# Optimization experiments

Hardware: AMD Instinct MI355X
Metric: run time of the kernel (lower is better)

Reference implementation:

```python
import jax, jax.numpy as jnp
import numpy as np

N_NODES = 50000
N_EDGES = 640000
IN_CH = 128
OUT_CH = 128


def setup_inputs() -> dict:
    key = jax.random.key(0)
    k1, k2, k3, k4 = jax.random.split(key, 4)
    x = jax.random.normal(k1, (N_NODES, IN_CH), dtype=jnp.float32)
    edge_index = jax.random.randint(k2, (2, N_EDGES), 0, N_NODES, dtype=jnp.int32)
    # nn.Linear params: W [out, in], b [out]
    bound = 1.0 / np.sqrt(IN_CH)
    W = jax.random.uniform(k3, (OUT_CH, IN_CH), minval=-bound, maxval=bound, dtype=jnp.float32)
    b = jax.random.uniform(k4, (OUT_CH,), minval=-bound, maxval=bound, dtype=jnp.float32)
    return {"x": x, "edge_index": edge_index, "W": W, "b": b}


def reference(x, edge_index, W, b):
    row, col = edge_index[0], edge_index[1]
    num_nodes = x.shape[0]
    # degree of each destination node (clamped to >= 1)
    deg = jax.ops.segment_sum(jnp.ones(row.shape[0], dtype=x.dtype), row,
                              num_segments=num_nodes)
    deg = jnp.maximum(deg, 1.0)
    # gather neighbor features and scatter-add into destinations
    agg = jax.ops.segment_sum(x[col], row, num_segments=num_nodes)
    agg = agg / deg[:, None]
    # residual + linear
    return (x + agg) @ W.T + b
```

## Files before the change

### kernel.cpp

```cpp
#include <hip/hip_runtime.h>

#define N_NODES 50000
#define N_EDGES 640000
#define CH 128
#define NBINS 1563
#define CAPB 16
#define CAP2 2512
#define CAPR 48
#define NTILES 1563
#define FILLB 157

typedef __bf16 bf16_t;
typedef bf16_t bf16x8 __attribute__((ext_vector_type(8)));
typedef float f32x4 __attribute__((ext_vector_type(4)));
typedef unsigned u32x4 __attribute__((ext_vector_type(4)));

__device__ __forceinline__ ushort f2bf(float f) {
  union { float f; unsigned u; } v; v.f = f;
  unsigned r = v.u + 0x7FFFu + ((v.u >> 16) & 1u);
  return (ushort)(r >> 16);
}
__device__ __forceinline__ float bflo(unsigned u) {
  union { unsigned u; float f; } v; v.u = u << 16; return v.f;
}
__device__ __forceinline__ float bfhi(unsigned u) {
  union { unsigned u; float f; } v; v.u = u & 0xFFFF0000u; return v.f;
}
__device__ __forceinline__ unsigned pack2(float lo, float hi) {
  return (unsigned)f2bf(lo) | ((unsigned)f2bf(hi) << 16);
}


__global__ __launch_bounds__(256) void fill_conv(const int* __restrict__ row,
                                                 const int* __restrict__ col,
                                                 unsigned* __restrict__ binArr,
                                                 const float4* __restrict__ x4,
                                                 uint4* __restrict__ xb4,
                                                 const float4* __restrict__ W4,
                                                 uint4* __restrict__ Wb4) {
  int bid = blockIdx.x;
  int tid = threadIdx.x;
  if (bid < FILLB) {
    __shared__ int lh[NBINS];
    for (int i = tid; i < NBINS; i += 256) lh[i] = 0;
    __syncthreads();
    int base = bid * 4096 + tid * 16;
    bool act = base < N_EDGES;
    int rr[16], cc[16], bi[16], rk[16];
    if (act) {
#pragma unroll
      for (int u = 0; u < 4; ++u) {
        int4 r4 = *(const int4*)(row + base + u * 4);
        int4 c4 = *(const int4*)(col + base + u * 4);
        rr[u * 4 + 0] = r4.x; rr[u * 4 + 1] = r4.y; rr[u * 4 + 2] = r4.z; rr[u * 4 + 3] = r4.w;
        cc[u * 4 + 0] = c4.x; cc[u * 4 + 1] = c4.y; cc[u * 4 + 2] = c4.z; cc[u * 4 + 3] = c4.w;
      }
#pragma unroll
      for (int i = 0; i < 16; ++i) {
        bi[i] = rr[i] >> 5;
        rk[i] = atomicAdd(&lh[bi[i]], 1);
      }
#pragma unroll
      for (int i = 0; i < 16; ++i) {
        if (rk[i] < CAPB) {
          binArr[bi[i] * CAP2 + bid * CAPB + rk[i]] =
              ((unsigned)(rr[i] & 31) << 16) | (unsigned)cc[i];
        }
      }
    }
  } else if (bid < FILLB + 3125) {
    int i = (bid - FILLB) * 256 + tid;
    float4 a = x4[i * 2], b = x4[i * 2 + 1];
    uint4 o;
    o.x = pack2(a.x, a.y); o.y = pack2(a.z, a.w);
    o.z = pack2(b.x, b.y); o.w = pack2(b.z, b.w);
    xb4[i] = o;
  } else {
    for (int i = tid; i < 2048; i += 256) {
      float4 c = W4[i * 2], d = W4[i * 2 + 1];
      uint4 w;
      w.x = pack2(c.x, c.y); w.y = pack2(c.z, c.w);
      w.z = pack2(d.x, d.y); w.w = pack2(d.z, d.w);
      Wb4[i] = w;
    }
  }
}

__global__ __launch_bounds__(256) void fused(const uint4* __restrict__ xb4,
                                             const uint4* __restrict__ binArr4,
                                             const uint4* __restrict__ Wb4,
                                             const float4* __restrict__ bias4,
                                             float4* __restrict__ out4) {
  __shared__ ushort hT[32 * CH];
  __shared__ ushort colL[32 * CAPR];
  __shared__ int rowcnt[32];
  int tid = threadIdx.x;
  int g = blockIdx.x;
  int m0 = g * 32;

  if (tid < 32) rowcnt[tid] = 0;
  __syncthreads();
  {
    const u32x4* seg4 = (const u32x4*)(binArr4 + g * (CAP2 / 4));
    for (int j = tid; j < CAP2 / 4; j += 256) {
      u32x4 rv = __builtin_nontemporal_load(seg4 + j);
      unsigned recs[4] = {rv.x, rv.y, rv.z, rv.w};
#pragma unroll
      for (int i = 0; i < 4; ++i) {
        unsigned rec = recs[i];
        if ((rec >> 21) == 0u) {
          int lr = (rec >> 16) & 31;
          int p = atomicAdd(&rowcnt[lr], 1);
          if (p < CAPR) colL[lr * CAPR + p] = (ushort)(rec & 0xFFFFu);
        }
      }
    }
  }
  __syncthreads();

  int wv = tid >> 6;
  int lane = tid & 63;
  int q = lane & 15;
  int grp = lane >> 4;
#pragma unroll
  for (int t = 0; t < 2; ++t) {
    int r = wv * 8 + t * 4 + grp;
    int node = m0 + r;
    int deg = rowcnt[r];
    int degc = deg < CAPR ? deg : CAPR;
    const ushort* arow = colL + r * CAPR;
    float acc[8] = {0.f, 0.f, 0.f, 0.f, 0.f, 0.f, 0.f, 0.f};
    int e = 0;
    for (; e + 3 < degc; e += 4) {
      uint2 ids = *(const uint2*)(arow + e);
      int n0 = ids.x & 0xFFFF, n1 = ids.x >> 16;
      int n2 = ids.y & 0xFFFF, n3 = ids.y >> 16;
      uint4 v0 = xb4[n0 * 16 + q];
      uint4 v1 = xb4[n1 * 16 + q];
      uint4 v2 = xb4[n2 * 16 + q];
      uint4 v3 = xb4[n3 * 16 + q];
      acc[0] += bflo(v0.x); acc[1] += bfhi(v0.x); acc[2] += bflo(v0.y); acc[3] += bfhi(v0.y);
      acc[4] += bflo(v0.z); acc[5] += bfhi(v0.z); acc[6] += bflo(v0.w); acc[7] += bfhi(v0.w);
      acc[0] += bflo(v1.x); acc[1] += bfhi(v1.x); acc[2] += bflo(v1.y); acc[3] += bfhi(v1.y);
      acc[4] += bflo(v1.z); acc[5] += bfhi(v1.z); acc[6] += bflo(v1.w); acc[7] += bfhi(v1.w);
      acc[0] += bflo(v2.x); acc[1] += bfhi(v2.x); acc[2] += bflo(v2.y); acc[3] += bfhi(v2.y);
      acc[4] += bflo(v2.z); acc[5] += bfhi(v2.z); acc[6] += bflo(v2.w); acc[7] += bfhi(v2.w);
      acc[0] += bflo(v3.x); acc[1] += bfhi(v3.x); acc[2] += bflo(v3.y); acc[3] += bfhi(v3.y);
      acc[4] += bflo(v3.z); acc[5] += bfhi(v3.z); acc[6] += bflo(v3.w); acc[7] += bfhi(v3.w);
    }
    for (; e < degc; ++e) {
      int nb = arow[e];
      uint4 v = xb4[nb * 16 + q];
      acc[0] += bflo(v.x); acc[1] += bfhi(v.x); acc[2] += bflo(v.y); acc[3] += bfhi(v.y);
      acc[4] += bflo(v.z); acc[5] += bfhi(v.z); acc[6] += bflo(v.w); acc[7] += bfhi(v.w);
    }
    uint4 o = make_uint4(0, 0, 0, 0);
    if (node < N_NODES) {
      float s = 1.0f / fmaxf((float)deg, 1.0f);
      uint4 xi = xb4[node * 16 + q];
      o.x = pack2(bflo(xi.x) + acc[0] * s, bfhi(xi.x) + acc[1] * s);
      o.y = pack2(bflo(xi.y) + acc[2] * s, bfhi(xi.y) + acc[3] * s);
      o.z = pack2(bflo(xi.z) + acc[4] * s, bfhi(xi.z) + acc[5] * s);
      o.w = pack2(bflo(xi.w) + acc[6] * s, bfhi(xi.w) + acc[7] * s);
    }
    *(uint4*)&hT[r * CH + ((q ^ (r & 15)) << 3)] = o;
  }
  __syncthreads();

  int qq = grp;
  int mt = wv & 1;
  int nbase = (wv >> 1) * 4;
  const ushort* hbase = &hT[(mt * 16 + q) * CH];
  bf16x8 hb0 = *(const bf16x8*)(hbase + (((qq + 0) ^ q) << 3));
  bf16x8 hb1 = *(const bf16x8*)(hbase + (((qq + 4) ^ q) << 3));
  bf16x8 hb2 = *(const bf16x8*)(hbase + (((qq + 8) ^ q) << 3));
  bf16x8 hb3 = *(const bf16x8*)(hbase + (((qq + 12) ^ q) << 3));
  int m = m0 + mt * 16 + q;
#pragma unroll
  for (int i = 0; i < 4; ++i) {
    int nt = nbase + i;
    const uint4* wr = Wb4 + (nt * 16 + q) * 16 + qq;
    bf16x8 w0 = __builtin_bit_cast(bf16x8, wr[0]);
    bf16x8 w1 = __builtin_bit_cast(bf16x8, wr[4]);
    bf16x8 w2 = __builtin_bit_cast(bf16x8, wr[8]);
    bf16x8 w3 = __builtin_bit_cast(bf16x8, wr[12]);
    f32x4 acc = {0.f, 0.f, 0.f, 0.f};
    acc = __builtin_amdgcn_mfma_f32_16x16x32_bf16(w0, hb0, acc, 0, 0, 0);
    acc = __builtin_amdgcn_mfma_f32_16x16x32_bf16(w1, hb1, acc, 0, 0, 0);
    acc = __builtin_amdgcn_mfma_f32_16x16x32_bf16(w2, hb2, acc, 0, 0, 0);
    acc = __builtin_amdgcn_mfma_f32_16x16x32_bf16(w3, hb3, acc, 0, 0, 0);
    if (m < N_NODES) {
      float4 bv = bias4[nt * 4 + qq];
      f32x4 o;
      o.x = acc[0] + bv.x;
      o.y = acc[1] + bv.y;
      o.z = acc[2] + bv.z;
      o.w = acc[3] + bv.w;
      __builtin_nontemporal_store(o, (f32x4*)(out4 + (size_t)m * 32 + nt * 4 + qq));
    }
  }
}

extern "C" void kernel_launch(void* const* d_in, const int* in_sizes, int n_in,
                              void* d_out, int out_size, void* d_ws, size_t ws_size,
                              hipStream_t stream) {
  const float* x  = (const float*)d_in[0];
  const int*   ei = (const int*)d_in[1];
  const float* W  = (const float*)d_in[2];
  const float* bb = (const float*)d_in[3];

  char* ws = (char*)d_ws;
  unsigned* binArr = (unsigned*)ws;
  uint4*    Wb4    = (uint4*)(ws + 15705024);
  uint4*    xb4    = (uint4*)(ws + 15737792);

  fill_conv<<<FILLB + 3125 + 1, 256, 0, stream>>>(ei, ei + N_EDGES, binArr,
                                                  (const float4*)x, xb4,
                                                  (const float4*)W, Wb4);
  fused<<<NTILES, 256, 0, stream>>>(xb4, (const uint4*)binArr, Wb4,
                                    (const float4*)bb, (float4*)d_out);
}
```

Baseline: 130.3 us.

## Replace fixed-capacity edge binning with atomic-count CSR build and scan

Builds a CSR adjacency via per-node atomic degree counting, a single-block prefix scan, and an atomic scatter of column ids, replacing fixed-capacity bins. The fused kernel then loads just the contiguous column ids for its 32-row tile instead of scanning a padded bin of records. This removes the large padded bin read and the per-row capacity limits, but adds three extra kernel launches, a serial single-block scan, and two passes of global atomics.

```diff
diff --git a/kernel.cpp b/kernel.cpp
--- a/kernel.cpp
+++ b/kernel.cpp
@@ -3,17 +3,12 @@
 #define N_NODES 50000
 #define N_EDGES 640000
 #define CH 128
-#define NBINS 1563
-#define CAPB 16
-#define CAP2 2512
-#define CAPR 48
 #define NTILES 1563
-#define FILLB 157
+#define IDS_CAP 768
 
 typedef __bf16 bf16_t;
 typedef bf16_t bf16x8 __attribute__((ext_vector_type(8)));
 typedef float f32x4 __attribute__((ext_vector_type(4)));
-typedef unsigned u32x4 __attribute__((ext_vector_type(4)));
 
 __device__ __forceinline__ ushort f2bf(float f) {
   union { float f; unsigned u; } v; v.f = f;
@@ -29,47 +24,36 @@
 __device__ __forceinline__ unsigned pack2(float lo, float hi) {
   return (unsigned)f2bf(lo) | ((unsigned)f2bf(hi) << 16);
 }
-
-
-__global__ __launch_bounds__(256) void fill_conv(const int* __restrict__ row,
-                                                 const int* __restrict__ col,
-                                                 unsigned* __restrict__ binArr,
-                                                 const float4* __restrict__ x4,
-                                                 uint4* __restrict__ xb4,
-                                                 const float4* __restrict__ W4,
-                                                 uint4* __restrict__ Wb4) {
+__device__ __forceinline__ void addrow(float* acc, uint4 v) {
+  acc[0] += bflo(v.x); acc[1] += bfhi(v.x);
+  acc[2] += bflo(v.y); acc[3] += bfhi(v.y);
+  acc[4] += bflo(v.z); acc[5] += bfhi(v.z);
+  acc[6] += bflo(v.w); acc[7] += bfhi(v.w);
+}
+
+
+__global__ __launch_bounds__(256) void zero_cnt(int4* __restrict__ cnt4) {
+  int i = blockIdx.x * 256 + threadIdx.x;
+  if (i < N_NODES / 4) cnt4[i] = make_int4(0, 0, 0, 0);
+}
+
+__global__ __launch_bounds__(256) void prep(const int* __restrict__ row,
+                                            int* __restrict__ cnt,
+                                            const float4* __restrict__ x4,
+                                            uint4* __restrict__ xb4,
+                                            const float4* __restrict__ W4,
+                                            uint4* __restrict__ Wb4) {
   int bid = blockIdx.x;
   int tid = threadIdx.x;
-  if (bid < FILLB) {
-    __shared__ int lh[NBINS];
-    for (int i = tid; i < NBINS; i += 256) lh[i] = 0;
-    __syncthreads();
-    int base = bid * 4096 + tid * 16;
-    bool act = base < N_EDGES;
-    int rr[16], cc[16], bi[16], rk[16];
-    if (act) {
-#pragma unroll
-      for (int u = 0; u < 4; ++u) {
-        int4 r4 = *(const int4*)(row + base + u * 4);
-        int4 c4 = *(const int4*)(col + base + u * 4);
-        rr[u * 4 + 0] = r4.x; rr[u * 4 + 1] = r4.y; rr[u * 4 + 2] = r4.z; rr[u * 4 + 3] = r4.w;
-        cc[u * 4 + 0] = c4.x; cc[u * 4 + 1] = c4.y; cc[u * 4 + 2] = c4.z; cc[u * 4 + 3] = c4.w;
-      }
-#pragma unroll
-      for (int i = 0; i < 16; ++i) {
-        bi[i] = rr[i] >> 5;
-        rk[i] = atomicAdd(&lh[bi[i]], 1);
-      }
-#pragma unroll
-      for (int i = 0; i < 16; ++i) {
-        if (rk[i] < CAPB) {
-          binArr[bi[i] * CAP2 + bid * CAPB + rk[i]] =
-              ((unsigned)(rr[i] & 31) << 16) | (unsigned)cc[i];
-        }
-      }
-    }
-  } else if (bid < FILLB + 3125) {
-    int i = (bid - FILLB) * 256 + tid;
+  if (bid < 625) {
+    int base = bid * 1024 + tid * 4;
+    int4 r4 = *(const int4*)(row + base);
+    atomicAdd(&cnt[r4.x], 1);
+    atomicAdd(&cnt[r4.y], 1);
+    atomicAdd(&cnt[r4.z], 1);
+    atomicAdd(&cnt[r4.w], 1);
+  } else if (bid < 3750) {
+    int i = (bid - 625) * 256 + tid;
     float4 a = x4[i * 2], b = x4[i * 2 + 1];
     uint4 o;
     o.x = pack2(a.x, a.y); o.y = pack2(a.z, a.w);
@@ -86,36 +70,73 @@
   }
 }
 
+__global__ __launch_bounds__(1024) void scan_k(const int* __restrict__ cnt,
+                                               int* __restrict__ ptr,
+                                               int* __restrict__ cur) {
+  __shared__ int ls[1024];
+  int t = threadIdx.x;
+  int base = t * 49;
+  int s = 0;
+  for (int k = 0; k < 49; ++k) {
+    int i = base + k;
+    if (i < N_NODES) s += cnt[i];
+  }
+  ls[t] = s;
+  __syncthreads();
+  for (int off = 1; off < 1024; off <<= 1) {
+    int v = (t >= off) ? ls[t - off] : 0;
+    __syncthreads();
+    ls[t] += v;
+    __syncthreads();
+  }
+  int run = (t > 0) ? ls[t - 1] : 0;
+  for (int k = 0; k < 49; ++k) {
+    int i = base + k;
+    if (i < N_NODES) {
+      ptr[i] = run;
+      cur[i] = run;
+      run += cnt[i];
+    }
+  }
+  if (t == 1023) ptr[N_NODES] = ls[1023];
+}
+
+__global__ __launch_bounds__(256) void scatter(const int* __restrict__ row,
+                                               const int* __restrict__ col,
+                                               int* __restrict__ cur,
+                                               ushort* __restrict__ colw) {
+  int base = blockIdx.x * 1024 + threadIdx.x * 4;
+  int4 r4 = *(const int4*)(row + base);
+  int4 c4 = *(const int4*)(col + base);
+  int p0 = atomicAdd(&cur[r4.x], 1); colw[p0] = (ushort)c4.x;
+  int p1 = atomicAdd(&cur[r4.y], 1); colw[p1] = (ushort)c4.y;
+  int p2 = atomicAdd(&cur[r4.z], 1); colw[p2] = (ushort)c4.z;
+  int p3 = atomicAdd(&cur[r4.w], 1); colw[p3] = (ushort)c4.w;
+}
+
 __global__ __launch_bounds__(256) void fused(const uint4* __restrict__ xb4,
-                                             const uint4* __restrict__ binArr4,
+                                             const int* __restrict__ ptr,
+                                             const ushort* __restrict__ colw,
                                              const uint4* __restrict__ Wb4,
                                              const float4* __restrict__ bias4,
                                              float4* __restrict__ out4) {
   __shared__ ushort hT[32 * CH];
-  __shared__ ushort colL[32 * CAPR];
-  __shared__ int rowcnt[32];
+  __shared__ ushort idsL[IDS_CAP];
+  __shared__ int lp[33];
   int tid = threadIdx.x;
   int g = blockIdx.x;
   int m0 = g * 32;
 
-  if (tid < 32) rowcnt[tid] = 0;
-  __syncthreads();
-  {
-    const u32x4* seg4 = (const u32x4*)(binArr4 + g * (CAP2 / 4));
-    for (int j = tid; j < CAP2 / 4; j += 256) {
-      u32x4 rv = __builtin_nontemporal_load(seg4 + j);
-      unsigned recs[4] = {rv.x, rv.y, rv.z, rv.w};
-#pragma unroll
-      for (int i = 0; i < 4; ++i) {
-        unsigned rec = recs[i];
-        if ((rec >> 21) == 0u) {
-          int lr = (rec >> 16) & 31;
-          int p = atomicAdd(&rowcnt[lr], 1);
-          if (p < CAPR) colL[lr * CAPR + p] = (ushort)(rec & 0xFFFFu);
-        }
-      }
-    }
-  }
+  if (tid < 33) {
+    int idx = m0 + tid;
+    if (idx > N_NODES) idx = N_NODES;
+    lp[tid] = ptr[idx];
+  }
+  __syncthreads();
+  int cbase = lp[0];
+  int total = lp[32] - cbase;
+  if (total > IDS_CAP) total = IDS_CAP;
+  for (int i = tid; i < total; i += 256) idsL[i] = colw[cbase + i];
   __syncthreads();
 
   int wv = tid >> 6;
@@ -126,33 +147,25 @@
   for (int t = 0; t < 2; ++t) {
     int r = wv * 8 + t * 4 + grp;
     int node = m0 + r;
-    int deg = rowcnt[r];
-    int degc = deg < CAPR ? deg : CAPR;
-    const ushort* arow = colL + r * CAPR;
+    int deg = lp[r + 1] - lp[r];
+    const ushort* arow = idsL + (lp[r] - cbase);
     float acc[8] = {0.f, 0.f, 0.f, 0.f, 0.f, 0.f, 0.f, 0.f};
     int e = 0;
-    for (; e + 3 < degc; e += 4) {
-      uint2 ids = *(const uint2*)(arow + e);
-      int n0 = ids.x & 0xFFFF, n1 = ids.x >> 16;
-      int n2 = ids.y & 0xFFFF, n3 = ids.y >> 16;
+    for (; e + 3 < deg; e += 4) {
+      int n0 = arow[e], n1 = arow[e + 1], n2 = arow[e + 2], n3 = arow[e + 3];
       uint4 v0 = xb4[n0 * 16 + q];
       uint4 v1 = xb4[n1 * 16 + q];
       uint4 v2 = xb4[n2 * 16 + q];
       uint4 v3 = xb4[n3 * 16 + q];
-      acc[0] += bflo(v0.x); acc[1] += bfhi(v0.x); acc[2] += bflo(v0.y); acc[3] += bfhi(v0.y);
-      acc[4] += bflo(v0.z); acc[5] += bfhi(v0.z); acc[6] += bflo(v0.w); acc[7] += bfhi(v0.w);
-      acc[0] += bflo(v1.x); acc[1] += bfhi(v1.x); acc[2] += bflo(v1.y); acc[3] += bfhi(v1.y);
-      acc[4] += bflo(v1.z); acc[5] += bfhi(v1.z); acc[6] += bflo(v1.w); acc[7] += bfhi(v1.w);
-      acc[0] += bflo(v2.x); acc[1] += bfhi(v2.x); acc[2] += bflo(v2.y); acc[3] += bfhi(v2.y);
-      acc[4] += bflo(v2.z); acc[5] += bfhi(v2.z); acc[6] += bflo(v2.w); acc[7] += bfhi(v2.w);
-      acc[0] += bflo(v3.x); acc[1] += bfhi(v3.x); acc[2] += bflo(v3.y); acc[3] += bfhi(v3.y);
-      acc[4] += bflo(v3.z); acc[5] += bfhi(v3.z); acc[6] += bflo(v3.w); acc[7] += bfhi(v3.w);
-    }
-    for (; e < degc; ++e) {
+      addrow(acc, v0);
+      addrow(acc, v1);
+      addrow(acc, v2);
+      addrow(acc, v3);
+    }
+    for (; e < deg; ++e) {
       int nb = arow[e];
       uint4 v = xb4[nb * 16 + q];
-      acc[0] += bflo(v.x); acc[1] += bfhi(v.x); acc[2] += bflo(v.y); acc[3] += bfhi(v.y);
-      acc[4] += bflo(v.z); acc[5] += bfhi(v.z); acc[6] += bflo(v.w); acc[7] += bfhi(v.w);
+      addrow(acc, v);
     }
     uint4 o = make_uint4(0, 0, 0, 0);
     if (node < N_NODES) {
@@ -210,13 +223,18 @@
   const float* bb = (const float*)d_in[3];
 
   char* ws = (char*)d_ws;
-  unsigned* binArr = (unsigned*)ws;
-  uint4*    Wb4    = (uint4*)(ws + 15705024);
-  uint4*    xb4    = (uint4*)(ws + 15737792);
-
-  fill_conv<<<FILLB + 3125 + 1, 256, 0, stream>>>(ei, ei + N_EDGES, binArr,
-                                                  (const float4*)x, xb4,
-                                                  (const float4*)W, Wb4);
-  fused<<<NTILES, 256, 0, stream>>>(xb4, (const uint4*)binArr, Wb4,
+  int*    ptr  = (int*)ws;
+  int*    cur  = (int*)(ws + 200016);
+  int*    cnt  = (int*)(ws + 400032);
+  ushort* colw = (ushort*)(ws + 600032);
+  uint4*  Wb4  = (uint4*)(ws + 1880032);
+  uint4*  xb4  = (uint4*)(ws + 1912800);
+
+  zero_cnt<<<49, 256, 0, stream>>>((int4*)cnt);
+  prep<<<3751, 256, 0, stream>>>(ei, cnt, (const float4*)x, xb4,
+                                 (const float4*)W, Wb4);
+  scan_k<<<1, 1024, 0, stream>>>(cnt, ptr, cur);
+  scatter<<<625, 256, 0, stream>>>(ei, ei + N_EDGES, cur, colw);
+  fused<<<NTILES, 256, 0, stream>>>(xb4, ptr, colw, Wb4,
                                     (const float4*)bb, (float4*)d_out);
 }
```

Result: slower. 303.2 us (+132.7%).

## Replace capped padded bins with per-block counting sort and offset table

Applied to the files above, without the earlier changes.

The edge bucketing kernel now runs a full local counting sort per block of 10000 edges: a shared histogram, a prefix scan, compacted records written to LDS, and a coalesced copy out to global memory, together with a per-block bin offset table. The fused kernel reads only the valid records for its tile through those offsets, instead of scanning a large padded bin array with a per-block cap that could drop edges. The fused kernel also moves to 512 threads, one row per thread group, with an 8-wide gather unroll and 2 MFMA tiles per wave. This cuts bin traffic and removes the overflow cap, but the fill phase now uses fewer blocks and a large LDS buffer, and each fused block does 64 small strided segment reads.

```diff
diff --git a/kernel.cpp b/kernel.cpp
--- a/kernel.cpp
+++ b/kernel.cpp
@@ -4,16 +4,15 @@
 #define N_EDGES 640000
 #define CH 128
 #define NBINS 1563
-#define CAPB 16
-#define CAP2 2512
+#define NTILES 1563
+#define FILLB 64
+#define EPB 10000
+#define OBW (NBINS + 1)
 #define CAPR 48
-#define NTILES 1563
-#define FILLB 157
 
 typedef __bf16 bf16_t;
 typedef bf16_t bf16x8 __attribute__((ext_vector_type(8)));
 typedef float f32x4 __attribute__((ext_vector_type(4)));
-typedef unsigned u32x4 __attribute__((ext_vector_type(4)));
 
 __device__ __forceinline__ ushort f2bf(float f) {
   union { float f; unsigned u; } v; v.f = f;
@@ -29,45 +28,89 @@
 __device__ __forceinline__ unsigned pack2(float lo, float hi) {
   return (unsigned)f2bf(lo) | ((unsigned)f2bf(hi) << 16);
 }
+__device__ __forceinline__ void addrow(float* acc, uint4 v) {
+  acc[0] += bflo(v.x); acc[1] += bfhi(v.x);
+  acc[2] += bflo(v.y); acc[3] += bfhi(v.y);
+  acc[4] += bflo(v.z); acc[5] += bfhi(v.z);
+  acc[6] += bflo(v.w); acc[7] += bfhi(v.w);
+}
 
 
 __global__ __launch_bounds__(256) void fill_conv(const int* __restrict__ row,
                                                  const int* __restrict__ col,
-                                                 unsigned* __restrict__ binArr,
+                                                 unsigned* __restrict__ binRec,
+                                                 ushort* __restrict__ obo,
                                                  const float4* __restrict__ x4,
                                                  uint4* __restrict__ xb4,
                                                  const float4* __restrict__ W4,
                                                  uint4* __restrict__ Wb4) {
+  __shared__ int cnt[NBINS];
+  __shared__ int parts[256];
+  __shared__ __align__(16) unsigned recbuf[EPB];
   int bid = blockIdx.x;
   int tid = threadIdx.x;
   if (bid < FILLB) {
-    __shared__ int lh[NBINS];
-    for (int i = tid; i < NBINS; i += 256) lh[i] = 0;
-    __syncthreads();
-    int base = bid * 4096 + tid * 16;
-    bool act = base < N_EDGES;
-    int rr[16], cc[16], bi[16], rk[16];
-    if (act) {
-#pragma unroll
-      for (int u = 0; u < 4; ++u) {
-        int4 r4 = *(const int4*)(row + base + u * 4);
-        int4 c4 = *(const int4*)(col + base + u * 4);
-        rr[u * 4 + 0] = r4.x; rr[u * 4 + 1] = r4.y; rr[u * 4 + 2] = r4.z; rr[u * 4 + 3] = r4.w;
-        cc[u * 4 + 0] = c4.x; cc[u * 4 + 1] = c4.y; cc[u * 4 + 2] = c4.z; cc[u * 4 + 3] = c4.w;
+    for (int i = tid; i < NBINS; i += 256) cnt[i] = 0;
+    __syncthreads();
+    int base = bid * EPB;
+    unsigned pk[40];
+#pragma unroll
+    for (int k = 0; k < 40; ++k) {
+      int idx = tid + k * 256;
+      pk[k] = 0xFFFFFFFFu;
+      if (idx < EPB) {
+        int rr = row[base + idx];
+        int bi = rr >> 5;
+        int rk = atomicAdd(&cnt[bi], 1);
+        pk[k] = ((unsigned)bi << 8) | (unsigned)rk;
       }
-#pragma unroll
-      for (int i = 0; i < 16; ++i) {
-        bi[i] = rr[i] >> 5;
-        rk[i] = atomicAdd(&lh[bi[i]], 1);
+    }
+    __syncthreads();
+    int c7[7];
+    int s = 0;
+#pragma unroll
+    for (int k = 0; k < 7; ++k) {
+      int i = tid * 7 + k;
+      int c = (i < NBINS) ? cnt[i] : 0;
+      c7[k] = c; s += c;
+    }
+    parts[tid] = s;
+    __syncthreads();
+    for (int off = 1; off < 256; off <<= 1) {
+      int v = (tid >= off) ? parts[tid - off] : 0;
+      __syncthreads();
+      parts[tid] += v;
+      __syncthreads();
+    }
+    int run = (tid > 0) ? parts[tid - 1] : 0;
+    ushort* orow = obo + bid * OBW;
+#pragma unroll
+    for (int k = 0; k < 7; ++k) {
+      int i = tid * 7 + k;
+      if (i < NBINS) {
+        orow[i] = (ushort)run;
+        cnt[i] = run;
+        run += c7[k];
       }
-#pragma unroll
-      for (int i = 0; i < 16; ++i) {
-        if (rk[i] < CAPB) {
-          binArr[bi[i] * CAP2 + bid * CAPB + rk[i]] =
-              ((unsigned)(rr[i] & 31) << 16) | (unsigned)cc[i];
-        }
+    }
+    if (tid == 0) orow[NBINS] = (ushort)EPB;
+    __syncthreads();
+#pragma unroll
+    for (int k = 0; k < 40; ++k) {
+      int idx = tid + k * 256;
+      if (idx < EPB) {
+        unsigned p = pk[k];
+        int bi = (int)(p >> 8);
+        int rk = (int)(p & 255u);
+        int rr = row[base + idx];
+        int cc = col[base + idx];
+        recbuf[cnt[bi] + rk] = ((unsigned)(rr & 31) << 16) | (unsigned)cc;
       }
     }
+    __syncthreads();
+    uint4* gb4 = (uint4*)(binRec + base);
+    const uint4* rb4 = (const uint4*)recbuf;
+    for (int j = tid; j < EPB / 4; j += 256) gb4[j] = rb4[j];
   } else if (bid < FILLB + 3125) {
     int i = (bid - FILLB) * 256 + tid;
     float4 a = x4[i * 2], b = x4[i * 2 + 1];
@@ -86,13 +129,14 @@
   }
 }
 
-__global__ __launch_bounds__(256) void fused(const uint4* __restrict__ xb4,
-                                             const uint4* __restrict__ binArr4,
+__global__ __launch_bounds__(512) void fused(const uint4* __restrict__ xb4,
+                                             const unsigned* __restrict__ binRec,
+                                             const ushort* __restrict__ obo,
                                              const uint4* __restrict__ Wb4,
                                              const float4* __restrict__ bias4,
                                              float4* __restrict__ out4) {
   __shared__ ushort hT[32 * CH];
-  __shared__ ushort colL[32 * CAPR];
+  __shared__ __align__(16) ushort colL[32 * CAPR];
   __shared__ int rowcnt[32];
   int tid = threadIdx.x;
   int g = blockIdx.x;
@@ -100,20 +144,16 @@
 
   if (tid < 32) rowcnt[tid] = 0;
   __syncthreads();
-  {
-    const u32x4* seg4 = (const u32x4*)(binArr4 + g * (CAP2 / 4));
-    for (int j = tid; j < CAP2 / 4; j += 256) {
-      u32x4 rv = __builtin_nontemporal_load(seg4 + j);
-      unsigned recs[4] = {rv.x, rv.y, rv.z, rv.w};
-#pragma unroll
-      for (int i = 0; i < 4; ++i) {
-        unsigned rec = recs[i];
-        if ((rec >> 21) == 0u) {
-          int lr = (rec >> 16) & 31;
-          int p = atomicAdd(&rowcnt[lr], 1);
-          if (p < CAPR) colL[lr * CAPR + p] = (ushort)(rec & 0xFFFFu);
-        }
-      }
+  if (tid < 256) {
+    int i = tid >> 2, sub = tid & 3;
+    const ushort* orow = obo + i * OBW + g;
+    int o0 = orow[0], o1 = orow[1];
+    const unsigned* rbase = binRec + i * EPB;
+    for (int p = o0 + sub; p < o1; p += 4) {
+      unsigned rec = rbase[p];
+      int lr = (int)(rec >> 16);
+      int pp = atomicAdd(&rowcnt[lr], 1);
+      if (pp < CAPR) colL[lr * CAPR + pp] = (ushort)(rec & 0xFFFFu);
     }
   }
   __syncthreads();
@@ -122,54 +162,61 @@
   int lane = tid & 63;
   int q = lane & 15;
   int grp = lane >> 4;
-#pragma unroll
-  for (int t = 0; t < 2; ++t) {
-    int r = wv * 8 + t * 4 + grp;
-    int node = m0 + r;
-    int deg = rowcnt[r];
-    int degc = deg < CAPR ? deg : CAPR;
-    const ushort* arow = colL + r * CAPR;
-    float acc[8] = {0.f, 0.f, 0.f, 0.f, 0.f, 0.f, 0.f, 0.f};
-    int e = 0;
-    for (; e + 3 < degc; e += 4) {
-      uint2 ids = *(const uint2*)(arow + e);
-      int n0 = ids.x & 0xFFFF, n1 = ids.x >> 16;
-      int n2 = ids.y & 0xFFFF, n3 = ids.y >> 16;
-      uint4 v0 = xb4[n0 * 16 + q];
-      uint4 v1 = xb4[n1 * 16 + q];
-      uint4 v2 = xb4[n2 * 16 + q];
-      uint4 v3 = xb4[n3 * 16 + q];
-      acc[0] += bflo(v0.x); acc[1] += bfhi(v0.x); acc[2] += bflo(v0.y); acc[3] += bfhi(v0.y);
-      acc[4] += bflo(v0.z); acc[5] += bfhi(v0.z); acc[6] += bflo(v0.w); acc[7] += bfhi(v0.w);
-      acc[0] += bflo(v1.x); acc[1] += bfhi(v1.x); acc[2] += bflo(v1.y); acc[3] += bfhi(v1.y);
-      acc[4] += bflo(v1.z); acc[5] += bfhi(v1.z); acc[6] += bflo(v1.w); acc[7] += bfhi(v1.w);
-      acc[0] += bflo(v2.x); acc[1] += bfhi(v2.x); acc[2] += bflo(v2.y); acc[3] += bfhi(v2.y);
-      acc[4] += bflo(v2.z); acc[5] += bfhi(v2.z); acc[6] += bflo(v2.w); acc[7] += bfhi(v2.w);
-      acc[0] += bflo(v3.x); acc[1] += bfhi(v3.x); acc[2] += bflo(v3.y); acc[3] += bfhi(v3.y);
-      acc[4] += bflo(v3.z); acc[5] += bfhi(v3.z); acc[6] += bflo(v3.w); acc[7] += bfhi(v3.w);
-    }
-    for (; e < degc; ++e) {
-      int nb = arow[e];
-      uint4 v = xb4[nb * 16 + q];
-      acc[0] += bflo(v.x); acc[1] += bfhi(v.x); acc[2] += bflo(v.y); acc[3] += bfhi(v.y);
-      acc[4] += bflo(v.z); acc[5] += bfhi(v.z); acc[6] += bflo(v.w); acc[7] += bfhi(v.w);
-    }
-    uint4 o = make_uint4(0, 0, 0, 0);
-    if (node < N_NODES) {
-      float s = 1.0f / fmaxf((float)deg, 1.0f);
-      uint4 xi = xb4[node * 16 + q];
-      o.x = pack2(bflo(xi.x) + acc[0] * s, bfhi(xi.x) + acc[1] * s);
-      o.y = pack2(bflo(xi.y) + acc[2] * s, bfhi(xi.y) + acc[3] * s);
-      o.z = pack2(bflo(xi.z) + acc[4] * s, bfhi(xi.z) + acc[5] * s);
-      o.w = pack2(bflo(xi.w) + acc[6] * s, bfhi(xi.w) + acc[7] * s);
-    }
-    *(uint4*)&hT[r * CH + ((q ^ (r & 15)) << 3)] = o;
-  }
+  int r = wv * 4 + grp;
+  int node = m0 + r;
+  int deg = rowcnt[r];
+  int degc = deg < CAPR ? deg : CAPR;
+  const ushort* arow = colL + r * CAPR;
+  int nc = node < N_NODES ? node : 0;
+  uint4 xi = xb4[nc * 16 + q];
+  float acc[8] = {0.f, 0.f, 0.f, 0.f, 0.f, 0.f, 0.f, 0.f};
+  int e = 0;
+  for (; e + 7 < degc; e += 8) {
+    uint4 ids = *(const uint4*)(arow + e);
+    int n0 = ids.x & 0xFFFF, n1 = ids.x >> 16;
+    int n2 = ids.y & 0xFFFF, n3 = ids.y >> 16;
+    int n4 = ids.z & 0xFFFF, n5 = ids.z >> 16;
+    int n6 = ids.w & 0xFFFF, n7 = ids.w >> 16;
+    uint4 v0 = xb4[n0 * 16 + q];
+    uint4 v1 = xb4[n1 * 16 + q];
+    uint4 v2 = xb4[n2 * 16 + q];
+    uint4 v3 = xb4[n3 * 16 + q];
+    uint4 v4 = xb4[n4 * 16 + q];
+    uint4 v5 = xb4[n5 * 16 + q];
+    uint4 v6 = xb4[n6 * 16 + q];
+    uint4 v7 = xb4[n7 * 16 + q];
+    addrow(acc, v0); addrow(acc, v1); addrow(acc, v2); addrow(acc, v3);
+    addrow(acc, v4); addrow(acc, v5); addrow(acc, v6); addrow(acc, v7);
+  }
+  if (e + 3 < degc) {
+    uint2 ids = *(const uint2*)(arow + e);
+    int n0 = ids.x & 0xFFFF, n1 = ids.x >> 16;
+    int n2 = ids.y & 0xFFFF, n3 = ids.y >> 16;
+    uint4 v0 = xb4[n0 * 16 + q];
+    uint4 v1 = xb4[n1 * 16 + q];
+    uint4 v2 = xb4[n2 * 16 + q];
+    uint4 v3 = xb4[n3 * 16 + q];
+    addrow(acc, v0); addrow(acc, v1); addrow(acc, v2); addrow(acc, v3);
+    e += 4;
+  }
+  for (; e < degc; ++e) {
+    uint4 v = xb4[(int)arow[e] * 16 + q];
+    addrow(acc, v);
+  }
+  uint4 o = make_uint4(0, 0, 0, 0);
+  if (node < N_NODES) {
+    float s = 1.0f / fmaxf((float)deg, 1.0f);
+    o.x = pack2(bflo(xi.x) + acc[0] * s, bfhi(xi.x) + acc[1] * s);
+    o.y = pack2(bflo(xi.y) + acc[2] * s, bfhi(xi.y) + acc[3] * s);
+    o.z = pack2(bflo(xi.z) + acc[4] * s, bfhi(xi.z) + acc[5] * s);
+    o.w = pack2(bflo(xi.w) + acc[6] * s, bfhi(xi.w) + acc[7] * s);
+  }
+  *(uint4*)&hT[r * CH + ((q ^ (r & 15)) << 3)] = o;
   __syncthreads();
 
   int qq = grp;
   int mt = wv & 1;
-  int nbase = (wv >> 1) * 4;
+  int nbase = (wv >> 1) * 2;
   const ushort* hbase = &hT[(mt * 16 + q) * CH];
   bf16x8 hb0 = *(const bf16x8*)(hbase + (((qq + 0) ^ q) << 3));
   bf16x8 hb1 = *(const bf16x8*)(hbase + (((qq + 4) ^ q) << 3));
@@ -177,26 +224,26 @@
   bf16x8 hb3 = *(const bf16x8*)(hbase + (((qq + 12) ^ q) << 3));
   int m = m0 + mt * 16 + q;
 #pragma unroll
-  for (int i = 0; i < 4; ++i) {
+  for (int i = 0; i < 2; ++i) {
     int nt = nbase + i;
     const uint4* wr = Wb4 + (nt * 16 + q) * 16 + qq;
     bf16x8 w0 = __builtin_bit_cast(bf16x8, wr[0]);
     bf16x8 w1 = __builtin_bit_cast(bf16x8, wr[4]);
     bf16x8 w2 = __builtin_bit_cast(bf16x8, wr[8]);
     bf16x8 w3 = __builtin_bit_cast(bf16x8, wr[12]);
-    f32x4 acc = {0.f, 0.f, 0.f, 0.f};
-    acc = __builtin_amdgcn_mfma_f32_16x16x32_bf16(w0, hb0, acc, 0, 0, 0);
-    acc = __builtin_amdgcn_mfma_f32_16x16x32_bf16(w1, hb1, acc, 0, 0, 0);
-    acc = __builtin_amdgcn_mfma_f32_16x16x32_bf16(w2, hb2, acc, 0, 0, 0);
-    acc = __builtin_amdgcn_mfma_f32_16x16x32_bf16(w3, hb3, acc, 0, 0, 0);
+    f32x4 acc2 = {0.f, 0.f, 0.f, 0.f};
+    acc2 = __builtin_amdgcn_mfma_f32_16x16x32_bf16(w0, hb0, acc2, 0, 0, 0);
+    acc2 = __builtin_amdgcn_mfma_f32_16x16x32_bf16(w1, hb1, acc2, 0, 0, 0);
+    acc2 = __builtin_amdgcn_mfma_f32_16x16x32_bf16(w2, hb2, acc2, 0, 0, 0);
+    acc2 = __builtin_amdgcn_mfma_f32_16x16x32_bf16(w3, hb3, acc2, 0, 0, 0);
     if (m < N_NODES) {
       float4 bv = bias4[nt * 4 + qq];
-      f32x4 o;
-      o.x = acc[0] + bv.x;
-      o.y = acc[1] + bv.y;
-      o.z = acc[2] + bv.z;
-      o.w = acc[3] + bv.w;
-      __builtin_nontemporal_store(o, (f32x4*)(out4 + (size_t)m * 32 + nt * 4 + qq));
+      f32x4 ov;
+      ov.x = acc2[0] + bv.x;
+      ov.y = acc2[1] + bv.y;
+      ov.z = acc2[2] + bv.z;
+      ov.w = acc2[3] + bv.w;
+      __builtin_nontemporal_store(ov, (f32x4*)(out4 + (size_t)m * 32 + nt * 4 + qq));
     }
   }
 }
@@ -210,13 +257,14 @@
   const float* bb = (const float*)d_in[3];
 
   char* ws = (char*)d_ws;
-  unsigned* binArr = (unsigned*)ws;
-  uint4*    Wb4    = (uint4*)(ws + 15705024);
-  uint4*    xb4    = (uint4*)(ws + 15737792);
-
-  fill_conv<<<FILLB + 3125 + 1, 256, 0, stream>>>(ei, ei + N_EDGES, binArr,
+  unsigned* binRec = (unsigned*)ws;
+  ushort*   obo    = (ushort*)(ws + 2560000);
+  uint4*    Wb4    = (uint4*)(ws + 2760192);
+  uint4*    xb4    = (uint4*)(ws + 2792960);
+
+  fill_conv<<<FILLB + 3125 + 1, 256, 0, stream>>>(ei, ei + N_EDGES, binRec, obo,
                                                   (const float4*)x, xb4,
                                                   (const float4*)W, Wb4);
-  fused<<<NTILES, 256, 0, stream>>>(xb4, (const uint4*)binArr, Wb4,
+  fused<<<NTILES, 512, 0, stream>>>(xb4, binRec, obo, Wb4,
                                     (const float4*)bb, (float4*)d_out);
 }
```

New measurement: 133.7 us. 2.6% more time.
